# Optimization experiments

Hardware: AMD Instinct MI355X
Metric: run time of the kernel (lower is better)

Reference implementation:

```python
import jax, jax.numpy as jnp
import numpy as np

ND, ED, HD, L, K = 128, 64, 256, 4, 24   # node_dim, edge_dim(num_rbf), hidden_dim, num_layers, max_neighbors
CUTOFF = 8.0
N = 2048  # n_atoms


def _silu(x):
    return x * jax.nn.sigmoid(x)


def _lattice(lengths, angles):
    a, b, c = lengths[0], lengths[1], lengths[2]
    deg = jnp.asarray(np.pi / 180.0, lengths.dtype)
    al, be, ga = angles[0] * deg, angles[1] * deg, angles[2] * deg
    lx = a
    xy = b * jnp.cos(ga)
    xz = c * jnp.cos(be)
    ly = b * jnp.sin(ga)
    yz = (b * c * jnp.cos(al) - xy * xz) / ly
    lz = jnp.sqrt(c ** 2 - xz ** 2 - yz ** 2)
    z = jnp.zeros((), lengths.dtype)
    return jnp.stack([jnp.stack([lx, z, z]), jnp.stack([xy, ly, z]), jnp.stack([xz, yz, lz])])


def _rbf(d):
    centers = jnp.linspace(0.0, CUTOFF, ED)
    widths = jnp.full((ED,), CUTOFF / ED)
    d = d[..., None]
    g = jnp.exp(-(d - centers) ** 2 / (2.0 * widths ** 2))
    cv = 0.5 * (jnp.cos(d * jnp.pi / CUTOFF) + 1.0) * (d < CUTOFF).astype(d.dtype)
    return g * cv


def _forward(atom_types, frac_coords, lengths, angles, timesteps, emb, tW, tb,
             eW1, eb1, eW2, eb2, nW1, nb1, nW2, nb2, cW1, cb1, cW2, cb2):
    n = frac_coords.shape[0]
    lattice = _lattice(lengths, angles)            # [3,3]
    cart = frac_coords @ lattice                   # [n,3]

    # ---- vectorized periodic neighbor graph (replaces host triple loop) ----
    shifts = jnp.asarray(np.array([[i, j, k] for i in (-1, 0, 1) for j in (-1, 0, 1) for k in (-1, 0, 1)],
                                  dtype=np.float32))
    sv = shifts @ lattice                          # [27,3]
    p = cart[None, :, :] + sv[:, None, :]          # [27,n,3] shifted atom positions
    # squared distances without materializing [27,n,n,3]
    d2 = (p * p).sum(-1)[:, :, None] + (cart * cart).sum(-1)[None, None, :] \
         - 2.0 * jnp.einsum('snk,mk->snm', p, cart)      # [27, n_j, n_i]
    dist = jnp.sqrt(jnp.maximum(d2, 1e-12))
    cand = jnp.where((dist < CUTOFF) & (dist > 0.01), dist, jnp.inf)
    cand = cand.reshape(27 * n, n).T               # [n_i, 27*n_j]; flat f = s*n + j
    _, idx = jax.lax.top_k(-cand, K)               # K smallest distances per atom i
    d_k = jnp.take_along_axis(cand, idx, axis=1)   # [n,K]
    dst = (idx % n).reshape(-1)                    # neighbor atom j (edge_list = [i, j])
    src = jnp.repeat(jnp.arange(n), K)             # center atom i
    valid = jnp.isfinite(d_k).reshape(-1)
    m = valid.astype(jnp.float32)[:, None]         # [E,1] pad mask
    d_e = jnp.where(valid, d_k.reshape(-1), 0.0)
    edge_attr = _rbf(d_e)                          # [E, ED]

    # ---- EGNN stack ----
    nf = emb[atom_types] + timesteps @ tW + tb     # [n, ND]
    coords = cart
    seg = lambda x, i: jax.ops.segment_sum(x, i, num_segments=n)
    for l in range(L):
        ef = jnp.concatenate([nf[src], nf[dst], edge_attr], axis=-1)   # [E, 2*ND+ED]
        msg = _silu(_silu(ef @ eW1[l] + eb1[l]) @ eW2[l] + eb2[l])     # [E, HD]
        aggr = seg(msg * m, dst)                                       # [n, HD]
        nf = nf + _silu(jnp.concatenate([nf, aggr], axis=-1) @ nW1[l] + nb1[l]) @ nW2[l] + nb2[l]
        w = _silu(msg @ cW1[l] + cb1[l]) @ cW2[l] + cb2[l]             # [E,1]
        cd = coords[src] - coords[dst]
        cd = cd / (jnp.linalg.norm(cd, axis=-1, keepdims=True) + 1e-8)
        coords = coords + seg(w * cd * m, dst)
    return nf, coords


def setup_inputs() -> dict:
    key = jax.random.key(0)
    ks = jax.random.split(key, 16)
    pr = lambda k, shape: jax.random.normal(k, shape, jnp.float32) * 0.02
    return dict(
        atom_types=jax.random.randint(ks[0], (N,), 0, 100),
        frac_coords=jax.random.uniform(ks[1], (N, 3), jnp.float32),
        lengths=jnp.ones((3,), jnp.float32) * 12.0,
        angles=jnp.ones((3,), jnp.float32) * 90.0,
        timesteps=jax.random.normal(ks[2], (N, 128), jnp.float32),
        emb=pr(ks[3], (100, ND)),
        tW=pr(ks[4], (128, ND)), tb=jnp.zeros((ND,), jnp.float32),
        eW1=pr(ks[5], (L, 2 * ND + ED, HD)), eb1=jnp.zeros((L, HD), jnp.float32),
        eW2=pr(ks[6], (L, HD, HD)), eb2=jnp.zeros((L, HD), jnp.float32),
        nW1=pr(ks[7], (L, ND + HD, HD)), nb1=jnp.zeros((L, HD), jnp.float32),
        nW2=pr(ks[8], (L, HD, ND)), nb2=jnp.zeros((L, ND), jnp.float32),
        cW1=pr(ks[9], (L, HD, HD // 2)), cb1=jnp.zeros((L, HD // 2), jnp.float32),
        cW2=pr(ks[10], (L, HD // 2, 1)), cb2=jnp.zeros((L, 1), jnp.float32),
    )


def reference(atom_types, frac_coords, lengths, angles, timesteps, emb, tW, tb,
              eW1, eb1, eW2, eb2, nW1, nb1, nW2, nb2, cW1, cb1, cW2, cb2):
    return _forward(atom_types, frac_coords, lengths, angles, timesteps, emb, tW, tb,
                    eW1, eb1, eW2, eb2, nW1, nb1, nW2, nb2, cW1, cb1, cW2, cb2)
```

## Files before the change

### kernel.cpp

```cpp
#include <hip/hip_runtime.h>
#include <math.h>

#define NA 2048
#define KN 24
#define NE (NA*KN)
#define NDIM 128
#define EDIM 64
#define HDIM 256
#define NLAYER 4
#define MAXDEG 256

typedef __attribute__((ext_vector_type(8))) short bf16x8;
typedef __attribute__((ext_vector_type(4))) float f32x4;

__device__ __forceinline__ float siluf(float x) { return x / (1.0f + expf(-x)); }
__device__ __forceinline__ ushort f2b(float x) {
    unsigned u = __float_as_uint(x);
    return (ushort)((u + 0x7fffu + ((u >> 16) & 1u)) >> 16);
}
__device__ __forceinline__ float b2f(ushort h) { return __uint_as_float(((unsigned)h) << 16); }

__device__ __forceinline__ void gl_lds(const void* g, void* lds) {
    __builtin_amdgcn_global_load_lds(
        (const __attribute__((address_space(1))) unsigned int*)g,
        (__attribute__((address_space(3))) unsigned int*)lds, 16, 0, 0);
}

struct Lat { float lx, xy, xz, ly, yz, lz; };

__device__ __forceinline__ Lat make_lattice(const float* lengths, const float* angles) {
    const float deg = 0.017453292519943295f;
    float a = lengths[0], b = lengths[1], c = lengths[2];
    float al = angles[0]*deg, be = angles[1]*deg, ga = angles[2]*deg;
    Lat L;
    L.lx = a;
    L.xy = b * cosf(ga);
    L.xz = c * cosf(be);
    L.ly = b * sinf(ga);
    L.yz = (b*c*cosf(al) - L.xy*L.xz) / L.ly;
    L.lz = sqrtf(c*c - L.xz*L.xz - L.yz*L.yz);
    return L;
}

__global__ void setup_kernel(const float* __restrict__ frac, const float* __restrict__ lengths,
                             const float* __restrict__ angles, float* __restrict__ cart,
                             float* __restrict__ cxg, float* __restrict__ cyg,
                             float* __restrict__ czg, float* __restrict__ sv,
                             int* __restrict__ ccnt) {
    int i = blockIdx.x*blockDim.x + threadIdx.x;
    Lat L = make_lattice(lengths, angles);
    if (i < NA) {
        float f0 = frac[i*3], f1 = frac[i*3+1], f2 = frac[i*3+2];
        float x = f0*L.lx + f1*L.xy + f2*L.xz;
        float y = f1*L.ly + f2*L.yz;
        float z = f2*L.lz;
        cart[i*3+0] = x; cart[i*3+1] = y; cart[i*3+2] = z;
        cxg[i] = x; cyg[i] = y; czg[i] = z;
        ccnt[i] = 0;
    }
    if (i < 27) {
        float s0 = (float)(i/9 - 1), s1 = (float)((i/3)%3 - 1), s2 = (float)(i%3 - 1);
        sv[i*3+0] = s0*L.lx + s1*L.xy + s2*L.xz;
        sv[i*3+1] = s1*L.ly + s2*L.yz;
        sv[i*3+2] = s2*L.lz;
    }
}

__global__ __launch_bounds__(64) void knn_kernel(
        const float* __restrict__ cxg, const float* __restrict__ cyg,
        const float* __restrict__ czg, const float* __restrict__ lengths,
        const float* __restrict__ angles, const float* __restrict__ sv,
        int* __restrict__ dstl, ushort* __restrict__ rbf16,
        int* __restrict__ ccnt, int* __restrict__ cedg) {
    __shared__ float sd2L[16][64];
    __shared__ int   sfL[16][64];
    const int lane = threadIdx.x;
    const int i = blockIdx.x;
    Lat L = make_lattice(lengths, angles);
    const float deg = 0.017453292519943295f;
    const bool ortho = fabsf(cosf(angles[0]*deg)) < 1e-6f &&
                       fabsf(cosf(angles[1]*deg)) < 1e-6f &&
                       fabsf(cosf(angles[2]*deg)) < 1e-6f;
    const float cx = cxg[i], cy = cyg[i], cz = czg[i];
    const float invlx = 1.0f/L.lx, invly = 1.0f/L.ly, invlz = 1.0f/L.lz;
    float R = 2.8f;
    int mycnt = 0, cnt = 0;
    bool flatm = false;
    for (int attempt = 0; attempt < 8; ++attempt) {
        const float R2 = R*R;
        mycnt = 0;
        flatm = !ortho || (attempt == 7);
        if (!flatm) {
#pragma unroll 2
            for (int j0 = 0; j0 < NA; j0 += 64) {
                const int j = j0 + lane;
                const float dx = cxg[j] - cx, dy = cyg[j] - cy, dz = czg[j] - cz;
                const float kx = rintf(dx*invlx), ky = rintf(dy*invly), kz = rintf(dz*invlz);
                const float ex = dx - (kx*L.lx + ky*L.xy + kz*L.xz);
                const float ey = dy - (ky*L.ly + kz*L.yz);
                const float ez = dz - kz*L.lz;
                const float d2 = fmaf(ex,ex,fmaf(ey,ey,ez*ez));
                if (d2 < R2 && d2 > 1e-4f) {
                    const int s = (1-(int)kx)*9 + (1-(int)ky)*3 + (1-(int)kz);
                    if (mycnt < 16) { sd2L[mycnt][lane] = d2; sfL[mycnt][lane] = (s<<11) + j; }
                    ++mycnt;
                }
            }
            if (__ballot(mycnt > 16)) {
                flatm = true;
            } else {
                int tot = mycnt;
                for (int off = 32; off > 0; off >>= 1) tot += __shfl_xor(tot, off, 64);
                cnt = tot;
            }
        }
        if (flatm) {
            cnt = 0;
            for (int s = 0; s < 27; ++s) {
                const float svx = sv[s*3], svy = sv[s*3+1], svz = sv[s*3+2];
                for (int j0 = 0; j0 < NA; j0 += 64) {
                    const int j = j0 + lane;
                    const float ex = cxg[j] + svx - cx;
                    const float ey = cyg[j] + svy - cy;
                    const float ez = czg[j] + svz - cz;
                    const float d2 = fmaf(ex,ex,fmaf(ey,ey,ez*ez));
                    const bool hit = (d2 < R2) && (d2 > 1e-4f);
                    const unsigned long long m = __ballot(hit);
                    const int rank = __popcll(m & ((1ull<<lane)-1ull));
                    const int slot = cnt + rank;
                    if (hit && slot < 1024) { sd2L[slot>>6][slot&63] = d2; sfL[slot>>6][slot&63] = (s<<11)+j; }
                    cnt += __popcll(m);
                }
            }
            cnt = min(cnt, 1024);
        }
        if (cnt >= KN) break;
        R = fminf(R*1.6f, flatm ? 8.0f : 5.9f);
    }
    int vq;
    if (flatm) vq = (lane < cnt) ? min(16, ((cnt - 1 - lane) >> 6) + 1) : 0;
    else       vq = mycnt;
    unsigned long long key[16];
#pragma unroll
    for (int q = 0; q < 16; ++q) {
        const float d2v = sd2L[q][lane];
        const int fl = sfL[q][lane];
        const unsigned long long kk = ((unsigned long long)__float_as_uint(d2v) << 20)
                                    | ((unsigned long long)(unsigned)fl << 4) | (unsigned)q;
        key[q] = (q < vq) ? kk : ~0ull;
    }
    float der[KN];
    for (int k = 0; k < KN; ++k) {
        unsigned long long lm = key[0];
#pragma unroll
        for (int q = 1; q < 16; ++q) lm = key[q] < lm ? key[q] : lm;
        for (int off = 32; off > 0; off >>= 1) {
            unsigned long long o = __shfl_xor(lm, off, 64);
            lm = o < lm ? o : lm;
        }
        der[k] = sqrtf(__uint_as_float((unsigned)(lm >> 20)));
        if (lane == 0) {
            const int jn = (int)((lm >> 4) & 2047u);
            dstl[i*KN + k] = jn;
            const int slot = atomicAdd(&ccnt[jn], 1);
            if (slot < MAXDEG) cedg[(size_t)jn*MAXDEG + slot] = i*KN + k;
        }
#pragma unroll
        for (int q = 0; q < 16; ++q) if (key[q] == lm) key[q] = ~0ull;
    }
    const float center = (8.0f/63.0f) * (float)lane;
    for (int k = 0; k < KN; ++k) {
        const float d = der[k];
        const float diff = d - center;
        const float g = expf(diff*diff * -32.0f);
        const float cv = 0.5f * (cosf(d * (float)(M_PI/8.0)) + 1.0f);
        rbf16[(size_t)(i*KN + k)*EDIM + lane] = f2b(g * cv);
    }
}

__global__ void csort_kernel(const int* __restrict__ ccnt, int* __restrict__ cedg) {
    const int j = blockIdx.x*4 + (threadIdx.x >> 6);
    const int lane = threadIdx.x & 63;
    const int cnt = min(ccnt[j], MAXDEG);
    if (cnt <= 64) {
        int v = (lane < cnt) ? cedg[(size_t)j*MAXDEG + lane] : 0x7FFFFFFF;
#pragma unroll
        for (int k = 2; k <= 64; k <<= 1) {
#pragma unroll
            for (int s = k >> 1; s > 0; s >>= 1) {
                int o = __shfl_xor(v, s, 64);
                const bool up = ((lane & k) == 0);
                const bool lowhalf = ((lane & s) == 0);
                v = ((lowhalf == up) ? min(v, o) : max(v, o));
            }
        }
        if (lane < cnt) cedg[(size_t)j*MAXDEG + lane] = v;
    } else if (lane == 0) {
        int* L = cedg + (size_t)j*MAXDEG;
        for (int a = 1; a < cnt; ++a) {
            int v = L[a]; int b = a - 1;
            while (b >= 0 && L[b] > v) { L[b+1] = L[b]; --b; }
            L[b+1] = v;
        }
    }
}

__global__ void nf_init_kernel(const int* __restrict__ atom_types, const float* __restrict__ ts,
                               const float* __restrict__ emb, const float* __restrict__ tW,
                               const float* __restrict__ tb, float* __restrict__ nf,
                               ushort* __restrict__ nf16) {
    int i = blockIdx.x, c = threadIdx.x;
    float acc = emb[atom_types[i]*NDIM + c] + tb[c];
    for (int kk = 0; kk < 128; ++kk) acc += ts[i*128 + kk] * tW[kk*NDIM + c];
    nf[i*NDIM + c] = acc;
    nf16[i*NDIM + c] = f2b(acc);
}

__global__ void wprep_all(const float* __restrict__ eW1, const float* __restrict__ eW2,
                          const float* __restrict__ cW1, const float* __restrict__ nW1,
                          const float* __restrict__ nW2,
                          ushort* __restrict__ eW1t, ushort* __restrict__ eW2t,
                          ushort* __restrict__ cW1t, ushort* __restrict__ nW1t,
                          ushort* __restrict__ nW2t) {
    __shared__ float tile[64][65];
    const int b = blockIdx.x;
    const float* W; ushort* Wt; int Kk, Nn, rel;
    if (b < 80)       { W = eW1; Wt = eW1t; Kk = 320; Nn = 256; rel = b; }
    else if (b < 144) { W = eW2; Wt = eW2t; Kk = 256; Nn = 256; rel = b - 80; }
    else if (b < 176) { W = cW1; Wt = cW1t; Kk = 256; Nn = 128; rel = b - 144; }
    else if (b < 272) { W = nW1; Wt = nW1t; Kk = 384; Nn = 256; rel = b - 176; }
    else              { W = nW2; Wt = nW2t; Kk = 256; Nn = 128; rel = b - 272; }
    const int kt = Kk >> 6, nt = Nn >> 6, per = kt*nt;
    const int l = rel / per, r2 = rel - l*per;
    const int k0 = (r2 / nt) * 64, n0 = (r2 - (r2/nt)*nt) * 64;
    const float* Wl = W + (size_t)l*Kk*Nn;
    ushort* Wtl = Wt + (size_t)l*Kk*Nn;
    const int tr = threadIdx.x >> 6, tc = threadIdx.x & 63;
#pragma unroll
    for (int q = 0; q < 16; ++q) {
        const int k = q*4 + tr;
        tile[k][tc] = Wl[(size_t)(k0 + k)*Nn + n0 + tc];
    }
    __syncthreads();
#pragma unroll
    for (int q = 0; q < 16; ++q) {
        const int n = q*4 + tr;
        Wtl[(size_t)(n0 + n)*Kk + k0 + tc] = f2b(tile[tc][n]);
    }
}

__global__ __launch_bounds__(256) void edge_fused(
        const ushort* __restrict__ nf16, const int* __restrict__ dstl,
        const ushort* __restrict__ rbf16,
        const ushort* __restrict__ eW1t,
        const ushort* __restrict__ eW2t,
        const ushort* __restrict__ cW1t,
        const float* __restrict__ eb1, const float* __restrict__ eb2,
        const float* __restrict__ cb1, const float* __restrict__ cW2v,
        const float* __restrict__ cb2v,
        ushort* __restrict__ msg16, float* __restrict__ wvout) {
    __shared__ alignas(16) char R0[40960];
    __shared__ alignas(16) char R1[32768];
    __shared__ int sdst[64];
    __shared__ float wred[2][64];
    ushort* As = (ushort*)R0;
    ushort* Bs = (ushort*)(R0 + 8192);
    ushort* B2 = (ushort*)R1;
    ushort* Cs = (ushort*)R1;

    const int t = threadIdx.x, wave = t >> 6, lane = t & 63;
    const int row0 = blockIdx.x*64;
    if (t < 64) sdst[t] = dstl[row0 + t];
    __syncthreads();
    const int wr = (wave >> 1)*32;
    const int wcB = (wave & 1)*128;
    const int lr = lane & 15, g0 = lane >> 4;

    auto STAGEA = [&](int buf, int k0) {
        {
            const int r = wave*16 + (lane >> 2);
            const int g = (lane & 3) ^ ((r >> 1) & 3);
            const int kg = k0 + g*8;
            const int e = row0 + r;
            const ushort* gp;
            if (kg < NDIM)        gp = nf16 + (size_t)(e/KN)*NDIM + kg;
            else if (kg < 2*NDIM) gp = nf16 + (size_t)sdst[r]*NDIM + (kg - NDIM);
            else                  gp = rbf16 + (size_t)e*EDIM + (kg - 2*NDIM);
            gl_lds(gp, As + (size_t)buf*2048 + (wave*16)*32);
        }
#pragma unroll
        for (int q = 0; q < 4; ++q) {
            const int rowb = wave*64 + q*16 + (lane >> 2);
            const int g = (lane & 3) ^ ((rowb >> 1) & 3);
            gl_lds(eW1t + (size_t)rowb*320 + k0 + g*8,
                   Bs + (size_t)buf*8192 + (wave*64 + q*16)*32);
        }
    };
    f32x4 acc[2][8];
#pragma unroll
    for (int m = 0; m < 2; ++m)
#pragma unroll
        for (int n = 0; n < 8; ++n) acc[m][n] = (f32x4){0.f,0.f,0.f,0.f};
    STAGEA(0, 0);
    int cur = 0;
    for (int it = 0; it < 10; ++it) {
        if (it + 1 < 10) {
            STAGEA(cur ^ 1, (it + 1)*32);
            asm volatile("s_waitcnt vmcnt(5)" ::: "memory");
        } else {
            asm volatile("s_waitcnt vmcnt(0)" ::: "memory");
        }
        __builtin_amdgcn_sched_barrier(0);
        __builtin_amdgcn_s_barrier();
        __builtin_amdgcn_sched_barrier(0);
        bf16x8 af[2], bfr[8];
#pragma unroll
        for (int m = 0; m < 2; ++m) {
            const int rA = wr + m*16 + lr;
            af[m] = *reinterpret_cast<const bf16x8*>(&As[cur*2048 + rA*32 + ((g0 ^ ((rA>>1)&3)))*8]);
        }
#pragma unroll
        for (int n = 0; n < 8; ++n) {
            const int rB = wcB + n*16 + lr;
            bfr[n] = *reinterpret_cast<const bf16x8*>(&Bs[(size_t)cur*8192 + rB*32 + ((g0 ^ ((rB>>1)&3)))*8]);
        }
#pragma unroll
        for (int m = 0; m < 2; ++m)
#pragma unroll
            for (int n = 0; n < 8; ++n)
                acc[m][n] = __builtin_amdgcn_mfma_f32_16x16x32_bf16(af[m], bfr[n], acc[m][n], 0, 0, 0);
        asm volatile("s_waitcnt lgkmcnt(0)" ::: "memory");
        __builtin_amdgcn_sched_barrier(0);
        __builtin_amdgcn_s_barrier();
        __builtin_amdgcn_sched_barrier(0);
        cur ^= 1;
    }
#pragma unroll
    for (int n = 0; n < 8; ++n) {
        const int cc = wcB + n*16 + lr;
        const float b1 = eb1[cc];
#pragma unroll
        for (int m = 0; m < 2; ++m) {
#pragma unroll
            for (int j = 0; j < 4; ++j) {
                const int rr = wr + m*16 + g0*4 + j;
                const float x = siluf(acc[m][n][j] + b1);
                *(ushort*)(R0 + rr*512 + ((cc*2) ^ ((rr&7)<<4))) = f2b(x);
            }
        }
    }
    __syncthreads();

#pragma unroll
    for (int m = 0; m < 2; ++m)
#pragma unroll
        for (int n = 0; n < 8; ++n) acc[m][n] = (f32x4){0.f,0.f,0.f,0.f};
    auto STAGEB = [&](int buf, int k0) {
#pragma unroll
        for (int q = 0; q < 4; ++q) {
            const int rowb = wave*64 + q*16 + (lane >> 2);
            const int g = (lane & 3) ^ ((rowb >> 1) & 3);
            gl_lds(eW2t + (size_t)rowb*256 + k0 + g*8,
                   B2 + (size_t)buf*8192 + (wave*64 + q*16)*32);
        }
    };
    STAGEB(0, 0);
    cur = 0;
    for (int it = 0; it < 8; ++it) {
        if (it + 1 < 8) {
            STAGEB(cur ^ 1, (it + 1)*32);
            asm volatile("s_waitcnt vmcnt(4)" ::: "memory");
        } else {
            asm volatile("s_waitcnt vmcnt(0)" ::: "memory");
        }
        __builtin_amdgcn_sched_barrier(0);
        __builtin_amdgcn_s_barrier();
        __builtin_amdgcn_sched_barrier(0);
        bf16x8 af[2], bfr[8];
#pragma unroll
        for (int m = 0; m < 2; ++m) {
            const int rA = wr + m*16 + lr;
            const int kc = it*4 + g0;
            af[m] = *reinterpret_cast<const bf16x8*>(R0 + rA*512 + ((kc*16) ^ ((rA&7)<<4)));
        }
#pragma unroll
        for (int n = 0; n < 8; ++n) {
            const int rB = wcB + n*16 + lr;
            bfr[n] = *reinterpret_cast<const bf16x8*>(&B2[(size_t)cur*8192 + rB*32 + ((g0 ^ ((rB>>1)&3)))*8]);
        }
#pragma unroll
        for (int m = 0; m < 2; ++m)
#pragma unroll
            for (int n = 0; n < 8; ++n)
                acc[m][n] = __builtin_amdgcn_mfma_f32_16x16x32_bf16(af[m], bfr[n], acc[m][n], 0, 0, 0);
        asm volatile("s_waitcnt lgkmcnt(0)" ::: "memory");
        __builtin_amdgcn_sched_barrier(0);
        __builtin_amdgcn_s_barrier();
        __builtin_amdgcn_sched_barrier(0);
        cur ^= 1;
    }
#pragma unroll
    for (int n = 0; n < 8; ++n) {
        const int cc = wcB + n*16 + lr;
        const float b2 = eb2[cc];
#pragma unroll
        for (int m = 0; m < 2; ++m) {
#pragma unroll
            for (int j = 0; j < 4; ++j) {
                const int rr = wr + m*16 + g0*4 + j;
                const ushort h = f2b(siluf(acc[m][n][j] + b2));
                msg16[(size_t)(row0 + rr)*256 + cc] = h;
                *(ushort*)(R0 + rr*512 + ((cc*2) ^ ((rr&7)<<4))) = h;
            }
        }
    }
    __syncthreads();

    const int wcC = (wave & 1)*64;
    f32x4 acc3[2][4];
#pragma unroll
    for (int m = 0; m < 2; ++m)
#pragma unroll
        for (int n = 0; n < 4; ++n) acc3[m][n] = (f32x4){0.f,0.f,0.f,0.f};
    auto STAGEC = [&](int buf, int k0) {
#pragma unroll
        for (int q = 0; q < 2; ++q) {
            const int rowb = wave*32 + q*16 + (lane >> 2);
            const int g = (lane & 3) ^ ((rowb >> 1) & 3);
            gl_lds(cW1t + (size_t)rowb*256 + k0 + g*8,
                   Cs + (size_t)buf*4096 + (wave*32 + q*16)*32);
        }
    };
    STAGEC(0, 0);
    cur = 0;
    for (int it = 0; it < 8; ++it) {
        if (it + 1 < 8) {
            STAGEC(cur ^ 1, (it + 1)*32);
            asm volatile("s_waitcnt vmcnt(2)" ::: "memory");
        } else {
            asm volatile("s_waitcnt vmcnt(0)" ::: "memory");
        }
        __builtin_amdgcn_sched_barrier(0);
        __builtin_amdgcn_s_barrier();
        __builtin_amdgcn_sched_barrier(0);
        bf16x8 af[2], bfr[4];
#pragma unroll
        for (int m = 0; m < 2; ++m) {
            const int rA = wr + m*16 + lr;
            const int kc = it*4 + g0;
            af[m] = *reinterpret_cast<const bf16x8*>(R0 + rA*512 + ((kc*16) ^ ((rA&7)<<4)));
        }
#pragma unroll
        for (int n = 0; n < 4; ++n) {
            const int rB = wcC + n*16 + lr;
            bfr[n] = *reinterpret_cast<const bf16x8*>(&Cs[(size_t)cur*4096 + rB*32 + ((g0 ^ ((rB>>1)&3)))*8]);
        }
#pragma unroll
        for (int m = 0; m < 2; ++m)
#pragma unroll
            for (int n = 0; n < 4; ++n)
                acc3[m][n] = __builtin_amdgcn_mfma_f32_16x16x32_bf16(af[m], bfr[n], acc3[m][n], 0, 0, 0);
        asm volatile("s_waitcnt lgkmcnt(0)" ::: "memory");
        __builtin_amdgcn_sched_barrier(0);
        __builtin_amdgcn_s_barrier();
        __builtin_amdgcn_sched_barrier(0);
        cur ^= 1;
    }
    float part[2][4];
#pragma unroll
    for (int m = 0; m < 2; ++m)
#pragma unroll
        for (int j = 0; j < 4; ++j) part[m][j] = 0.0f;
#pragma unroll
    for (int n = 0; n < 4; ++n) {
        const int cc = wcC + n*16 + lr;
        const float bb = cb1[cc];
        const float cw = cW2v[cc];
#pragma unroll
        for (int m = 0; m < 2; ++m)
#pragma unroll
            for (int j = 0; j < 4; ++j)
                part[m][j] += siluf(acc3[m][n][j] + bb) * cw;
    }
#pragma unroll
    for (int off = 1; off < 16; off <<= 1)
#pragma unroll
        for (int m = 0; m < 2; ++m)
#pragma unroll
            for (int j = 0; j < 4; ++j)
                part[m][j] += __shfl_xor(part[m][j], off, 64);
    if (lr == 0) {
#pragma unroll
        for (int m = 0; m < 2; ++m)
#pragma unroll
            for (int j = 0; j < 4; ++j)
                wred[wave & 1][wr + m*16 + g0*4 + j] = part[m][j];
    }
    __syncthreads();
    if (t < 64) wvout[row0 + t] = wred[0][t] + wred[1][t] + cb2v[0];
}

template<int AMODE, int EPI>
__global__ __launch_bounds__(256) void bgemm_kernel(
        const ushort* __restrict__ A, const ushort* __restrict__ nf16,
        const ushort* __restrict__ aggr16, const ushort* __restrict__ Bt,
        const float* __restrict__ bias, const float* __restrict__ res,
        float* __restrict__ Cf, ushort* __restrict__ C16, int M, int Nn, int Kk) {
    __shared__ alignas(16) ushort As[2][128*32];
    __shared__ alignas(16) ushort Bs[2][128*32];
    const int t = threadIdx.x;
    const int wave = t >> 6, lane = t & 63;
    const int row0 = blockIdx.x*128, col0 = blockIdx.y*128;
    const int wr = (wave >> 1)*64, wc = (wave & 1)*64;
    const int lr = lane & 15, g0 = lane >> 4;

    auto STAGE = [&](int buf, int k0) {
#pragma unroll
        for (int q = 0; q < 4; ++q) {
            const int rbase = (q & 1)*64 + wave*16;
            const int r = rbase + (lane >> 2);
            const int g = (lane & 3) ^ ((r >> 1) & 3);
            const int kg = k0 + g*8;
            const int ldsbase = rbase * 32;
            if (q < 2) {
                const ushort* gp;
                if (AMODE == 0) {
                    gp = A + (size_t)(row0 + r)*Kk + kg;
                } else {
                    const int e = row0 + r;
                    if (kg < NDIM) gp = nf16 + (size_t)e*NDIM + kg;
                    else           gp = aggr16 + (size_t)e*HDIM + (kg - NDIM);
                }
                gl_lds(gp, &As[buf][ldsbase]);
            } else {
                gl_lds(Bt + (size_t)(col0 + r)*Kk + kg, &Bs[buf][ldsbase]);
            }
        }
    };

    f32x4 acc[4][4] = {};
    const int nk = Kk >> 5;
    STAGE(0, 0);
    int cur = 0;
    for (int it = 0; it < nk; ++it) {
        if (it + 1 < nk) {
            STAGE(cur ^ 1, (it + 1) << 5);
            asm volatile("s_waitcnt vmcnt(4)" ::: "memory");
        } else {
            asm volatile("s_waitcnt vmcnt(0)" ::: "memory");
        }
        __builtin_amdgcn_sched_barrier(0);
        __builtin_amdgcn_s_barrier();
        __builtin_amdgcn_sched_barrier(0);
        bf16x8 af[4], bfr[4];
#pragma unroll
        for (int m = 0; m < 4; ++m) {
            const int rA = wr + m*16 + lr;
            af[m] = *reinterpret_cast<const bf16x8*>(&As[cur][rA*32 + (g0 ^ ((rA>>1)&3))*8]);
        }
#pragma unroll
        for (int n = 0; n < 4; ++n) {
            const int rB = wc + n*16 + lr;
            bfr[n] = *reinterpret_cast<const bf16x8*>(&Bs[cur][rB*32 + (g0 ^ ((rB>>1)&3))*8]);
        }
#pragma unroll
        for (int m = 0; m < 4; ++m)
#pragma unroll
            for (int n = 0; n < 4; ++n)
                acc[m][n] = __builtin_amdgcn_mfma_f32_16x16x32_bf16(af[m], bfr[n], acc[m][n], 0, 0, 0);
        asm volatile("s_waitcnt lgkmcnt(0)" ::: "memory");
        __builtin_amdgcn_sched_barrier(0);
        __builtin_amdgcn_s_barrier();
        __builtin_amdgcn_sched_barrier(0);
        cur ^= 1;
    }

#pragma unroll
    for (int n = 0; n < 4; ++n) {
        const int cc = col0 + wc + n*16 + lr;
        const float bb = bias[cc];
#pragma unroll
        for (int m = 0; m < 4; ++m) {
#pragma unroll
            for (int j = 0; j < 4; ++j) {
                const int rr = row0 + wr + m*16 + (lane >> 4)*4 + j;
                float x = acc[m][n][j] + bb;
                if constexpr (EPI == 0) {
                    C16[(size_t)rr*Nn + cc] = f2b(siluf(x));
                } else {
                    x += res[(size_t)rr*Nn + cc];
                    Cf[(size_t)rr*Nn + cc] = x;
                    C16[(size_t)rr*Nn + cc] = f2b(x);
                }
            }
        }
    }
}

__global__ void aggr_kernel(const ushort* __restrict__ msg16, const int* __restrict__ ccnt,
                            const int* __restrict__ cedg, ushort* __restrict__ aggr16) {
    __shared__ int se[4][64];
    const int w = threadIdx.x >> 6, lane = threadIdx.x & 63;
    const int j = blockIdx.x*4 + w;
    const int cnt = min(ccnt[j], MAXDEG);
    se[w][lane] = (lane < cnt) ? cedg[(size_t)j*MAXDEG + lane] : 0;
    __syncthreads();
    const int c4 = lane*4;
    float s0 = 0, s1 = 0, s2 = 0, s3 = 0;
    const int lim = min(cnt, 64);
    for (int q = 0; q < lim; ++q) {
        const int e = se[w][q];
        ushort4 v = *reinterpret_cast<const ushort4*>(&msg16[(size_t)e*HDIM + c4]);
        s0 += b2f(v.x); s1 += b2f(v.y); s2 += b2f(v.z); s3 += b2f(v.w);
    }
    for (int q = 64; q < cnt; ++q) {
        const int e = cedg[(size_t)j*MAXDEG + q];
        ushort4 v = *reinterpret_cast<const ushort4*>(&msg16[(size_t)e*HDIM + c4]);
        s0 += b2f(v.x); s1 += b2f(v.y); s2 += b2f(v.z); s3 += b2f(v.w);
    }
    ushort4 o; o.x = f2b(s0); o.y = f2b(s1); o.z = f2b(s2); o.w = f2b(s3);
    *reinterpret_cast<ushort4*>(&aggr16[(size_t)j*HDIM + c4]) = o;
}

__global__ void coords_kernel(const float* __restrict__ cold, const float* __restrict__ wv,
                              const int* __restrict__ ccnt, const int* __restrict__ cedg,
                              float* __restrict__ cnew) {
    const int w = threadIdx.x >> 6, lane = threadIdx.x & 63;
    const int j = blockIdx.x*4 + w;
    const int cnt = min(ccnt[j], MAXDEG);
    const float jx = cold[j*3], jy = cold[j*3+1], jz = cold[j*3+2];
    float dx = 0, dy = 0, dz = 0;
    for (int q = lane; q < cnt; q += 64) {
        const int e = cedg[(size_t)j*MAXDEG + q];
        const int si = e / KN;
        const float ax = cold[si*3]   - jx;
        const float ay = cold[si*3+1] - jy;
        const float az = cold[si*3+2] - jz;
        const float inv = wv[e] / (sqrtf(ax*ax + ay*ay + az*az) + 1e-8f);
        dx += inv*ax; dy += inv*ay; dz += inv*az;
    }
    for (int off = 32; off > 0; off >>= 1) {
        dx += __shfl_xor(dx, off, 64);
        dy += __shfl_xor(dy, off, 64);
        dz += __shfl_xor(dz, off, 64);
    }
    if (lane == 0) {
        cnew[j*3]   = jx + dx;
        cnew[j*3+1] = jy + dy;
        cnew[j*3+2] = jz + dz;
    }
}

__global__ void copyout_kernel(const float* __restrict__ nf, const float* __restrict__ coords,
                               float* __restrict__ out) {
    int idx = blockIdx.x*256 + threadIdx.x;
    if (idx < NA*NDIM) out[idx] = nf[idx];
    else if (idx < NA*NDIM + NA*3) out[idx] = coords[idx - NA*NDIM];
}

extern "C" void kernel_launch(void* const* d_in, const int* in_sizes, int n_in,
                              void* d_out, int out_size, void* d_ws, size_t ws_size,
                              hipStream_t stream) {
    const int*   atom_types = (const int*)  d_in[0];
    const float* frac       = (const float*)d_in[1];
    const float* lengths    = (const float*)d_in[2];
    const float* angles     = (const float*)d_in[3];
    const float* timesteps  = (const float*)d_in[4];
    const float* emb        = (const float*)d_in[5];
    const float* tW         = (const float*)d_in[6];
    const float* tb         = (const float*)d_in[7];
    const float* eW1        = (const float*)d_in[8];
    const float* eb1        = (const float*)d_in[9];
    const float* eW2        = (const float*)d_in[10];
    const float* eb2        = (const float*)d_in[11];
    const float* nW1        = (const float*)d_in[12];
    const float* nb1        = (const float*)d_in[13];
    const float* nW2        = (const float*)d_in[14];
    const float* nb2        = (const float*)d_in[15];
    const float* cW1        = (const float*)d_in[16];
    const float* cb1        = (const float*)d_in[17];
    const float* cW2        = (const float*)d_in[18];
    const float* cb2        = (const float*)d_in[19];

    char* p = (char*)d_ws;
    auto alloc = [&](size_t bytes) { char* q = p; p += (bytes + 255) & ~(size_t)255; return q; };
    float*  sv    = (float*) alloc(81*4);
    float*  c0    = (float*) alloc((size_t)NA*3*4);
    float*  c1    = (float*) alloc((size_t)NA*3*4);
    float*  cxg   = (float*) alloc((size_t)NA*4);
    float*  cyg   = (float*) alloc((size_t)NA*4);
    float*  czg   = (float*) alloc((size_t)NA*4);
    float*  nf    = (float*) alloc((size_t)NA*NDIM*4);
    int*    dstl  = (int*)   alloc((size_t)NE*4);
    ushort* rbf16 = (ushort*)alloc((size_t)NE*EDIM*2);
    int*    ccnt  = (int*)   alloc((size_t)NA*4);
    int*    cedg  = (int*)   alloc((size_t)NA*MAXDEG*4);
    ushort* aggr16= (ushort*)alloc((size_t)NA*HDIM*2);
    ushort* t116  = (ushort*)alloc((size_t)NA*HDIM*2);
    float*  wv    = (float*) alloc((size_t)NE*4);
    ushort* nf16  = (ushort*)alloc((size_t)NA*NDIM*2);
    ushort* msg16 = (ushort*)alloc((size_t)NE*HDIM*2);
    ushort* eW1t  = (ushort*)alloc((size_t)NLAYER*(2*NDIM+EDIM)*HDIM*2);
    ushort* eW2t  = (ushort*)alloc((size_t)NLAYER*HDIM*HDIM*2);
    ushort* cW1t  = (ushort*)alloc((size_t)NLAYER*(HDIM/2)*HDIM*2);
    ushort* nW1t  = (ushort*)alloc((size_t)NLAYER*(NDIM+HDIM)*HDIM*2);
    ushort* nW2t  = (ushort*)alloc((size_t)NLAYER*HDIM*NDIM*2);

    setup_kernel<<<8, 256, 0, stream>>>(frac, lengths, angles, c0, cxg, cyg, czg, sv, ccnt);
    knn_kernel<<<NA, 64, 0, stream>>>(cxg, cyg, czg, lengths, angles, sv,
                                      dstl, rbf16, ccnt, cedg);
    csort_kernel<<<NA/4, 256, 0, stream>>>(ccnt, cedg);
    nf_init_kernel<<<NA, 128, 0, stream>>>(atom_types, timesteps, emb, tW, tb, nf, nf16);
    wprep_all<<<304, 256, 0, stream>>>(eW1, eW2, cW1, nW1, nW2,
                                       eW1t, eW2t, cW1t, nW1t, nW2t);

    float* cin = c0; float* cout = c1;
    for (int l = 0; l < NLAYER; ++l) {
        const float* eb1l = eb1 + (size_t)l*HDIM;
        const float* eb2l = eb2 + (size_t)l*HDIM;
        const float* nb1l = nb1 + (size_t)l*HDIM;
        const float* nb2l = nb2 + (size_t)l*NDIM;
        const float* cb1l = cb1 + (size_t)l*(HDIM/2);
        const float* cW2l = cW2 + (size_t)l*(HDIM/2);
        const float* cb2l = cb2 + (size_t)l;

        edge_fused<<<NE/64, 256, 0, stream>>>(
            nf16, dstl, rbf16,
            eW1t + (size_t)l*(2*NDIM+EDIM)*HDIM, eW2t + (size_t)l*HDIM*HDIM,
            cW1t + (size_t)l*(HDIM/2)*HDIM,
            eb1l, eb2l, cb1l, cW2l, cb2l, msg16, wv);
        aggr_kernel<<<NA/4, 256, 0, stream>>>(msg16, ccnt, cedg, aggr16);
        bgemm_kernel<2,0><<<dim3(NA/128, HDIM/128), 256, 0, stream>>>(
            nullptr, nf16, aggr16, nW1t + (size_t)l*(NDIM+HDIM)*HDIM, nb1l, nullptr,
            nullptr, t116, NA, HDIM, NDIM+HDIM);
        bgemm_kernel<0,2><<<dim3(NA/128, NDIM/128), 256, 0, stream>>>(
            t116, nullptr, nullptr, nW2t + (size_t)l*HDIM*NDIM, nb2l, nf,
            nf, nf16, NA, NDIM, HDIM);
        coords_kernel<<<NA/4, 256, 0, stream>>>(cin, wv, ccnt, cedg, cout);
        float* tmp = cin; cin = cout; cout = tmp;
    }
    copyout_kernel<<<(NA*NDIM + NA*3)/256, 256, 0, stream>>>(nf, cin, (float*)d_out);
}
```

Measured before the change: 418.1 us.

## Enlarge edge_fused tile to 96 edges and restructure LDS and staging

Raises the edge tile per block from 64 to 96 rows, so each wave computes three 16-row MFMA slabs and every weight tile loaded into LDS is reused across more edges. The LDS regions are remapped, and the first weight tile of the next GEMM stage is prefetched while the previous epilogue runs. msg16 is now written with coalesced 16-byte stores from the swizzled LDS tile instead of scattered 2-byte stores, and s_setprio is raised around the MFMA blocks. In exchange it uses more LDS and registers (possible occupancy loss), balances A-loads unevenly across waves, and launches fewer blocks.

After: 467.4 us. +11.8%, slower.

```diff
diff --git a/kernel.cpp b/kernel.cpp
--- a/kernel.cpp
+++ b/kernel.cpp
@@ -9,6 +9,7 @@
 #define HDIM 256
 #define NLAYER 4
 #define MAXDEG 256
+#define EB 96
 
 typedef __attribute__((ext_vector_type(8))) short bf16x8;
 typedef __attribute__((ext_vector_type(4))) float f32x4;
@@ -259,26 +260,29 @@
         const float* __restrict__ cb1, const float* __restrict__ cW2v,
         const float* __restrict__ cb2v,
         ushort* __restrict__ msg16, float* __restrict__ wvout) {
-    __shared__ alignas(16) char R0[40960];
+    __shared__ alignas(16) char R0[49152];
     __shared__ alignas(16) char R1[32768];
-    __shared__ int sdst[64];
-    __shared__ float wred[2][64];
-    ushort* As = (ushort*)R0;
-    ushort* Bs = (ushort*)(R0 + 8192);
+    ushort* Bs = (ushort*)R0;
+    int*    sdst = (int*)(R0 + 32768);
+    ushort* As = (ushort*)R1;
     ushort* B2 = (ushort*)R1;
     ushort* Cs = (ushort*)R1;
+    float*  wredp = (float*)R1;
 
     const int t = threadIdx.x, wave = t >> 6, lane = t & 63;
-    const int row0 = blockIdx.x*64;
-    if (t < 64) sdst[t] = dstl[row0 + t];
+    const int row0 = blockIdx.x*EB;
+    if (t < EB) sdst[t] = dstl[row0 + t];
     __syncthreads();
-    const int wr = (wave >> 1)*32;
+    const int wr = (wave >> 1)*48;
     const int wcB = (wave & 1)*128;
     const int lr = lane & 15, g0 = lane >> 4;
 
     auto STAGEA = [&](int buf, int k0) {
-        {
-            const int r = wave*16 + (lane >> 2);
+        const int na = (wave < 2) ? 2 : 1;
+        const int a0 = (wave < 2) ? wave*2 : wave + 2;
+        for (int q = 0; q < na; ++q) {
+            const int grp = a0 + q;
+            const int r = grp*16 + (lane >> 2);
             const int g = (lane & 3) ^ ((r >> 1) & 3);
             const int kg = k0 + g*8;
             const int e = row0 + r;
@@ -286,7 +290,7 @@
             if (kg < NDIM)        gp = nf16 + (size_t)(e/KN)*NDIM + kg;
             else if (kg < 2*NDIM) gp = nf16 + (size_t)sdst[r]*NDIM + (kg - NDIM);
             else                  gp = rbf16 + (size_t)e*EDIM + (kg - 2*NDIM);
-            gl_lds(gp, As + (size_t)buf*2048 + (wave*16)*32);
+            gl_lds(gp, As + (size_t)buf*3072 + grp*512);
         }
 #pragma unroll
         for (int q = 0; q < 4; ++q) {
@@ -296,9 +300,9 @@
                    Bs + (size_t)buf*8192 + (wave*64 + q*16)*32);
         }
     };
-    f32x4 acc[2][8];
-#pragma unroll
-    for (int m = 0; m < 2; ++m)
+    f32x4 acc[3][8];
+#pragma unroll
+    for (int m = 0; m < 3; ++m)
 #pragma unroll
         for (int n = 0; n < 8; ++n) acc[m][n] = (f32x4){0.f,0.f,0.f,0.f};
     STAGEA(0, 0);
@@ -306,41 +310,53 @@
     for (int it = 0; it < 10; ++it) {
         if (it + 1 < 10) {
             STAGEA(cur ^ 1, (it + 1)*32);
-            asm volatile("s_waitcnt vmcnt(5)" ::: "memory");
+            if (wave < 2) asm volatile("s_waitcnt vmcnt(6)" ::: "memory");
+            else          asm volatile("s_waitcnt vmcnt(5)" ::: "memory");
         } else {
             asm volatile("s_waitcnt vmcnt(0)" ::: "memory");
         }
         __builtin_amdgcn_sched_barrier(0);
         __builtin_amdgcn_s_barrier();
         __builtin_amdgcn_sched_barrier(0);
-        bf16x8 af[2], bfr[8];
-#pragma unroll
-        for (int m = 0; m < 2; ++m) {
+        bf16x8 af[3], bfr[8];
+#pragma unroll
+        for (int m = 0; m < 3; ++m) {
             const int rA = wr + m*16 + lr;
-            af[m] = *reinterpret_cast<const bf16x8*>(&As[cur*2048 + rA*32 + ((g0 ^ ((rA>>1)&3)))*8]);
+            af[m] = *reinterpret_cast<const bf16x8*>(&As[cur*3072 + rA*32 + ((g0 ^ ((rA>>1)&3)))*8]);
         }
 #pragma unroll
         for (int n = 0; n < 8; ++n) {
             const int rB = wcB + n*16 + lr;
             bfr[n] = *reinterpret_cast<const bf16x8*>(&Bs[(size_t)cur*8192 + rB*32 + ((g0 ^ ((rB>>1)&3)))*8]);
         }
-#pragma unroll
-        for (int m = 0; m < 2; ++m)
+        __builtin_amdgcn_s_setprio(1);
+#pragma unroll
+        for (int m = 0; m < 3; ++m)
 #pragma unroll
             for (int n = 0; n < 8; ++n)
                 acc[m][n] = __builtin_amdgcn_mfma_f32_16x16x32_bf16(af[m], bfr[n], acc[m][n], 0, 0, 0);
+        __builtin_amdgcn_s_setprio(0);
         asm volatile("s_waitcnt lgkmcnt(0)" ::: "memory");
         __builtin_amdgcn_sched_barrier(0);
         __builtin_amdgcn_s_barrier();
         __builtin_amdgcn_sched_barrier(0);
         cur ^= 1;
+    }
+    {
+#pragma unroll
+        for (int q = 0; q < 4; ++q) {
+            const int rowb = wave*64 + q*16 + (lane >> 2);
+            const int g = (lane & 3) ^ ((rowb >> 1) & 3);
+            gl_lds(eW2t + (size_t)rowb*256 + g*8,
+                   B2 + (wave*64 + q*16)*32);
+        }
     }
 #pragma unroll
     for (int n = 0; n < 8; ++n) {
         const int cc = wcB + n*16 + lr;
         const float b1 = eb1[cc];
 #pragma unroll
-        for (int m = 0; m < 2; ++m) {
+        for (int m = 0; m < 3; ++m) {
 #pragma unroll
             for (int j = 0; j < 4; ++j) {
                 const int rr = wr + m*16 + g0*4 + j;
@@ -352,7 +368,7 @@
     __syncthreads();
 
 #pragma unroll
-    for (int m = 0; m < 2; ++m)
+    for (int m = 0; m < 3; ++m)
 #pragma unroll
         for (int n = 0; n < 8; ++n) acc[m][n] = (f32x4){0.f,0.f,0.f,0.f};
     auto STAGEB = [&](int buf, int k0) {
@@ -364,7 +380,6 @@
                    B2 + (size_t)buf*8192 + (wave*64 + q*16)*32);
         }
     };
-    STAGEB(0, 0);
     cur = 0;
     for (int it = 0; it < 8; ++it) {
         if (it + 1 < 8) {
@@ -376,9 +391,9 @@
         __builtin_amdgcn_sched_barrier(0);
         __builtin_amdgcn_s_barrier();
         __builtin_amdgcn_sched_barrier(0);
-        bf16x8 af[2], bfr[8];
-#pragma unroll
-        for (int m = 0; m < 2; ++m) {
+        bf16x8 af[3], bfr[8];
+#pragma unroll
+        for (int m = 0; m < 3; ++m) {
             const int rA = wr + m*16 + lr;
             const int kc = it*4 + g0;
             af[m] = *reinterpret_cast<const bf16x8*>(R0 + rA*512 + ((kc*16) ^ ((rA&7)<<4)));
@@ -388,38 +403,47 @@
             const int rB = wcB + n*16 + lr;
             bfr[n] = *reinterpret_cast<const bf16x8*>(&B2[(size_t)cur*8192 + rB*32 + ((g0 ^ ((rB>>1)&3)))*8]);
         }
-#pragma unroll
-        for (int m = 0; m < 2; ++m)
+        __builtin_amdgcn_s_setprio(1);
+#pragma unroll
+        for (int m = 0; m < 3; ++m)
 #pragma unroll
             for (int n = 0; n < 8; ++n)
                 acc[m][n] = __builtin_amdgcn_mfma_f32_16x16x32_bf16(af[m], bfr[n], acc[m][n], 0, 0, 0);
+        __builtin_amdgcn_s_setprio(0);
         asm volatile("s_waitcnt lgkmcnt(0)" ::: "memory");
         __builtin_amdgcn_sched_barrier(0);
         __builtin_amdgcn_s_barrier();
         __builtin_amdgcn_sched_barrier(0);
         cur ^= 1;
+    }
+    {
+#pragma unroll
+        for (int q = 0; q < 2; ++q) {
+            const int rowb = wave*32 + q*16 + (lane >> 2);
+            const int g = (lane & 3) ^ ((rowb >> 1) & 3);
+            gl_lds(cW1t + (size_t)rowb*256 + g*8,
+                   Cs + (wave*32 + q*16)*32);
+        }
     }
 #pragma unroll
     for (int n = 0; n < 8; ++n) {
         const int cc = wcB + n*16 + lr;
         const float b2 = eb2[cc];
 #pragma unroll
-        for (int m = 0; m < 2; ++m) {
+        for (int m = 0; m < 3; ++m) {
 #pragma unroll
             for (int j = 0; j < 4; ++j) {
                 const int rr = wr + m*16 + g0*4 + j;
-                const ushort h = f2b(siluf(acc[m][n][j] + b2));
-                msg16[(size_t)(row0 + rr)*256 + cc] = h;
-                *(ushort*)(R0 + rr*512 + ((cc*2) ^ ((rr&7)<<4))) = h;
+                *(ushort*)(R0 + rr*512 + ((cc*2) ^ ((rr&7)<<4))) = f2b(siluf(acc[m][n][j] + b2));
             }
         }
     }
     __syncthreads();
 
     const int wcC = (wave & 1)*64;
-    f32x4 acc3[2][4];
-#pragma unroll
-    for (int m = 0; m < 2; ++m)
+    f32x4 acc3[3][4];
+#pragma unroll
+    for (int m = 0; m < 3; ++m)
 #pragma unroll
         for (int n = 0; n < 4; ++n) acc3[m][n] = (f32x4){0.f,0.f,0.f,0.f};
     auto STAGEC = [&](int buf, int k0) {
@@ -431,7 +455,6 @@
                    Cs + (size_t)buf*4096 + (wave*32 + q*16)*32);
         }
     };
-    STAGEC(0, 0);
     cur = 0;
     for (int it = 0; it < 8; ++it) {
         if (it + 1 < 8) {
@@ -443,9 +466,9 @@
         __builtin_amdgcn_sched_barrier(0);
         __builtin_amdgcn_s_barrier();
         __builtin_amdgcn_sched_barrier(0);
-        bf16x8 af[2], bfr[4];
-#pragma unroll
-        for (int m = 0; m < 2; ++m) {
+        bf16x8 af[3], bfr[4];
+#pragma unroll
+        for (int m = 0; m < 3; ++m) {
             const int rA = wr + m*16 + lr;
             const int kc = it*4 + g0;
             af[m] = *reinterpret_cast<const bf16x8*>(R0 + rA*512 + ((kc*16) ^ ((rA&7)<<4)));
@@ -455,20 +478,22 @@
             const int rB = wcC + n*16 + lr;
             bfr[n] = *reinterpret_cast<const bf16x8*>(&Cs[(size_t)cur*4096 + rB*32 + ((g0 ^ ((rB>>1)&3)))*8]);
         }
-#pragma unroll
-        for (int m = 0; m < 2; ++m)
+        __builtin_amdgcn_s_setprio(1);
+#pragma unroll
+        for (int m = 0; m < 3; ++m)
 #pragma unroll
             for (int n = 0; n < 4; ++n)
                 acc3[m][n] = __builtin_amdgcn_mfma_f32_16x16x32_bf16(af[m], bfr[n], acc3[m][n], 0, 0, 0);
+        __builtin_amdgcn_s_setprio(0);
         asm volatile("s_waitcnt lgkmcnt(0)" ::: "memory");
         __builtin_amdgcn_sched_barrier(0);
         __builtin_amdgcn_s_barrier();
         __builtin_amdgcn_sched_barrier(0);
         cur ^= 1;
     }
-    float part[2][4];
-#pragma unroll
-    for (int m = 0; m < 2; ++m)
+    float part[3][4];
+#pragma unroll
+    for (int m = 0; m < 3; ++m)
 #pragma unroll
         for (int j = 0; j < 4; ++j) part[m][j] = 0.0f;
 #pragma unroll
@@ -477,7 +502,7 @@
         const float bb = cb1[cc];
         const float cw = cW2v[cc];
 #pragma unroll
-        for (int m = 0; m < 2; ++m)
+        for (int m = 0; m < 3; ++m)
 #pragma unroll
             for (int j = 0; j < 4; ++j)
                 part[m][j] += siluf(acc3[m][n][j] + bb) * cw;
@@ -485,19 +510,27 @@
 #pragma unroll
     for (int off = 1; off < 16; off <<= 1)
 #pragma unroll
-        for (int m = 0; m < 2; ++m)
+        for (int m = 0; m < 3; ++m)
 #pragma unroll
             for (int j = 0; j < 4; ++j)
                 part[m][j] += __shfl_xor(part[m][j], off, 64);
     if (lr == 0) {
 #pragma unroll
-        for (int m = 0; m < 2; ++m)
+        for (int m = 0; m < 3; ++m)
 #pragma unroll
             for (int j = 0; j < 4; ++j)
-                wred[wave & 1][wr + m*16 + g0*4 + j] = part[m][j];
+                wredp[(wave & 1)*EB + wr + m*16 + g0*4 + j] = part[m][j];
     }
     __syncthreads();
-    if (t < 64) wvout[row0 + t] = wred[0][t] + wred[1][t] + cb2v[0];
+    if (t < EB) wvout[row0 + t] = wredp[t] + wredp[EB + t] + cb2v[0];
+#pragma unroll
+    for (int k = 0; k < 12; ++k) {
+        const int off = (t + k*256) * 16;
+        const int row = off >> 9;
+        const int cg = ((off >> 4) & 31) ^ (row & 7);
+        uint4 v = *reinterpret_cast<const uint4*>(R0 + off);
+        *reinterpret_cast<uint4*>(msg16 + (size_t)(row0 + row)*256 + cg*8) = v;
+    }
 }
 
 template<int AMODE, int EPI>
@@ -724,7 +757,7 @@
         const float* cW2l = cW2 + (size_t)l*(HDIM/2);
         const float* cb2l = cb2 + (size_t)l;
 
-        edge_fused<<<NE/64, 256, 0, stream>>>(
+        edge_fused<<<NE/EB, 256, 0, stream>>>(
             nf16, dstl, rbf16,
             eW1t + (size_t)l*(2*NDIM+EDIM)*HDIM, eW2t + (size_t)l*HDIM*HDIM,
             cW1t + (size_t)l*(HDIM/2)*HDIM,
```

## Prefetch next GEMM weights early, coalesce msg stores, fuse aggr and coords kernels

Applied to the files above, without the earlier changes.

In the fused edge kernel, the first weight tiles for the second and third GEMMs are now issued right after the previous GEMM loop, before the epilogue runs. This lets the global loads overlap with the SiLU/bf16 conversion. The message tile is written to global memory with coalesced 16-byte stores from the swizzled LDS copy, replacing scattered 2-byte stores. MFMA blocks are wrapped in s_setprio, and the aggregation and coordinate-update kernels are merged into one node kernel that reuses the edge list cached in LDS, removing a launch per layer. The risk is that weight prefetches into R1/Cs could overlap buffers still being read, which is a correctness hazard if the aliasing is wrong.

Result: faster. 407.4 us (-2.6%).

```diff
diff --git a/kernel.cpp b/kernel.cpp
--- a/kernel.cpp
+++ b/kernel.cpp
@@ -9,6 +9,7 @@
 #define HDIM 256
 #define NLAYER 4
 #define MAXDEG 256
+#define EB 64
 
 typedef __attribute__((ext_vector_type(8))) short bf16x8;
 typedef __attribute__((ext_vector_type(4))) float f32x4;
@@ -269,8 +270,8 @@
     ushort* Cs = (ushort*)R1;
 
     const int t = threadIdx.x, wave = t >> 6, lane = t & 63;
-    const int row0 = blockIdx.x*64;
-    if (t < 64) sdst[t] = dstl[row0 + t];
+    const int row0 = blockIdx.x*EB;
+    if (t < EB) sdst[t] = dstl[row0 + t];
     __syncthreads();
     const int wr = (wave >> 1)*32;
     const int wcB = (wave & 1)*128;
@@ -324,16 +325,27 @@
             const int rB = wcB + n*16 + lr;
             bfr[n] = *reinterpret_cast<const bf16x8*>(&Bs[(size_t)cur*8192 + rB*32 + ((g0 ^ ((rB>>1)&3)))*8]);
         }
+        __builtin_amdgcn_s_setprio(1);
 #pragma unroll
         for (int m = 0; m < 2; ++m)
 #pragma unroll
             for (int n = 0; n < 8; ++n)
                 acc[m][n] = __builtin_amdgcn_mfma_f32_16x16x32_bf16(af[m], bfr[n], acc[m][n], 0, 0, 0);
+        __builtin_amdgcn_s_setprio(0);
         asm volatile("s_waitcnt lgkmcnt(0)" ::: "memory");
         __builtin_amdgcn_sched_barrier(0);
         __builtin_amdgcn_s_barrier();
         __builtin_amdgcn_sched_barrier(0);
         cur ^= 1;
+    }
+    {
+#pragma unroll
+        for (int q = 0; q < 4; ++q) {
+            const int rowb = wave*64 + q*16 + (lane >> 2);
+            const int g = (lane & 3) ^ ((rowb >> 1) & 3);
+            gl_lds(eW2t + (size_t)rowb*256 + g*8,
+                   B2 + (wave*64 + q*16)*32);
+        }
     }
 #pragma unroll
     for (int n = 0; n < 8; ++n) {
@@ -364,7 +376,6 @@
                    B2 + (size_t)buf*8192 + (wave*64 + q*16)*32);
         }
     };
-    STAGEB(0, 0);
     cur = 0;
     for (int it = 0; it < 8; ++it) {
         if (it + 1 < 8) {
@@ -388,16 +399,27 @@
             const int rB = wcB + n*16 + lr;
             bfr[n] = *reinterpret_cast<const bf16x8*>(&B2[(size_t)cur*8192 + rB*32 + ((g0 ^ ((rB>>1)&3)))*8]);
         }
+        __builtin_amdgcn_s_setprio(1);
 #pragma unroll
         for (int m = 0; m < 2; ++m)
 #pragma unroll
             for (int n = 0; n < 8; ++n)
                 acc[m][n] = __builtin_amdgcn_mfma_f32_16x16x32_bf16(af[m], bfr[n], acc[m][n], 0, 0, 0);
+        __builtin_amdgcn_s_setprio(0);
         asm volatile("s_waitcnt lgkmcnt(0)" ::: "memory");
         __builtin_amdgcn_sched_barrier(0);
         __builtin_amdgcn_s_barrier();
         __builtin_amdgcn_sched_barrier(0);
         cur ^= 1;
+    }
+    {
+#pragma unroll
+        for (int q = 0; q < 2; ++q) {
+            const int rowb = wave*32 + q*16 + (lane >> 2);
+            const int g = (lane & 3) ^ ((rowb >> 1) & 3);
+            gl_lds(cW1t + (size_t)rowb*256 + g*8,
+                   Cs + (wave*32 + q*16)*32);
+        }
     }
 #pragma unroll
     for (int n = 0; n < 8; ++n) {
@@ -408,9 +430,7 @@
 #pragma unroll
             for (int j = 0; j < 4; ++j) {
                 const int rr = wr + m*16 + g0*4 + j;
-                const ushort h = f2b(siluf(acc[m][n][j] + b2));
-                msg16[(size_t)(row0 + rr)*256 + cc] = h;
-                *(ushort*)(R0 + rr*512 + ((cc*2) ^ ((rr&7)<<4))) = h;
+                *(ushort*)(R0 + rr*512 + ((cc*2) ^ ((rr&7)<<4))) = f2b(siluf(acc[m][n][j] + b2));
             }
         }
     }
@@ -431,7 +451,6 @@
                    Cs + (size_t)buf*4096 + (wave*32 + q*16)*32);
         }
     };
-    STAGEC(0, 0);
     cur = 0;
     for (int it = 0; it < 8; ++it) {
         if (it + 1 < 8) {
@@ -455,11 +474,13 @@
             const int rB = wcC + n*16 + lr;
             bfr[n] = *reinterpret_cast<const bf16x8*>(&Cs[(size_t)cur*4096 + rB*32 + ((g0 ^ ((rB>>1)&3)))*8]);
         }
+        __builtin_amdgcn_s_setprio(1);
 #pragma unroll
         for (int m = 0; m < 2; ++m)
 #pragma unroll
             for (int n = 0; n < 4; ++n)
                 acc3[m][n] = __builtin_amdgcn_mfma_f32_16x16x32_bf16(af[m], bfr[n], acc3[m][n], 0, 0, 0);
+        __builtin_amdgcn_s_setprio(0);
         asm volatile("s_waitcnt lgkmcnt(0)" ::: "memory");
         __builtin_amdgcn_sched_barrier(0);
         __builtin_amdgcn_s_barrier();
@@ -497,7 +518,15 @@
                 wred[wave & 1][wr + m*16 + g0*4 + j] = part[m][j];
     }
     __syncthreads();
-    if (t < 64) wvout[row0 + t] = wred[0][t] + wred[1][t] + cb2v[0];
+    if (t < EB) wvout[row0 + t] = wred[0][t] + wred[1][t] + cb2v[0];
+#pragma unroll
+    for (int k = 0; k < 8; ++k) {
+        const int off = (t + k*256) * 16;
+        const int row = off >> 9;
+        const int cg = ((off >> 4) & 31) ^ (row & 7);
+        uint4 v = *reinterpret_cast<const uint4*>(R0 + off);
+        *reinterpret_cast<uint4*>(msg16 + (size_t)(row0 + row)*256 + cg*8) = v;
+    }
 }
 
 template<int AMODE, int EPI>
@@ -597,8 +626,10 @@
     }
 }
 
-__global__ void aggr_kernel(const ushort* __restrict__ msg16, const int* __restrict__ ccnt,
-                            const int* __restrict__ cedg, ushort* __restrict__ aggr16) {
+__global__ void node_kernel(const ushort* __restrict__ msg16, const float* __restrict__ cold,
+                            const float* __restrict__ wv, const int* __restrict__ ccnt,
+                            const int* __restrict__ cedg,
+                            ushort* __restrict__ aggr16, float* __restrict__ cnew) {
     __shared__ int se[4][64];
     const int w = threadIdx.x >> 6, lane = threadIdx.x & 63;
     const int j = blockIdx.x*4 + w;
@@ -620,18 +651,10 @@
     }
     ushort4 o; o.x = f2b(s0); o.y = f2b(s1); o.z = f2b(s2); o.w = f2b(s3);
     *reinterpret_cast<ushort4*>(&aggr16[(size_t)j*HDIM + c4]) = o;
-}
-
-__global__ void coords_kernel(const float* __restrict__ cold, const float* __restrict__ wv,
-                              const int* __restrict__ ccnt, const int* __restrict__ cedg,
-                              float* __restrict__ cnew) {
-    const int w = threadIdx.x >> 6, lane = threadIdx.x & 63;
-    const int j = blockIdx.x*4 + w;
-    const int cnt = min(ccnt[j], MAXDEG);
     const float jx = cold[j*3], jy = cold[j*3+1], jz = cold[j*3+2];
     float dx = 0, dy = 0, dz = 0;
     for (int q = lane; q < cnt; q += 64) {
-        const int e = cedg[(size_t)j*MAXDEG + q];
+        const int e = (q < 64) ? se[w][q] : cedg[(size_t)j*MAXDEG + q];
         const int si = e / KN;
         const float ax = cold[si*3]   - jx;
         const float ay = cold[si*3+1] - jy;
@@ -724,19 +747,18 @@
         const float* cW2l = cW2 + (size_t)l*(HDIM/2);
         const float* cb2l = cb2 + (size_t)l;
 
-        edge_fused<<<NE/64, 256, 0, stream>>>(
+        edge_fused<<<NE/EB, 256, 0, stream>>>(
             nf16, dstl, rbf16,
             eW1t + (size_t)l*(2*NDIM+EDIM)*HDIM, eW2t + (size_t)l*HDIM*HDIM,
             cW1t + (size_t)l*(HDIM/2)*HDIM,
             eb1l, eb2l, cb1l, cW2l, cb2l, msg16, wv);
-        aggr_kernel<<<NA/4, 256, 0, stream>>>(msg16, ccnt, cedg, aggr16);
+        node_kernel<<<NA/4, 256, 0, stream>>>(msg16, cin, wv, ccnt, cedg, aggr16, cout);
         bgemm_kernel<2,0><<<dim3(NA/128, HDIM/128), 256, 0, stream>>>(
             nullptr, nf16, aggr16, nW1t + (size_t)l*(NDIM+HDIM)*HDIM, nb1l, nullptr,
             nullptr, t116, NA, HDIM, NDIM+HDIM);
         bgemm_kernel<0,2><<<dim3(NA/128, NDIM/128), 256, 0, stream>>>(
             t116, nullptr, nullptr, nW2t + (size_t)l*HDIM*NDIM, nb2l, nf,
             nf, nf16, NA, NDIM, HDIM);
-        coords_kernel<<<NA/4, 256, 0, stream>>>(cin, wv, ccnt, cedg, cout);
         float* tmp = cin; cin = cout; cout = tmp;
     }
     copyout_kernel<<<(NA*NDIM + NA*3)/256, 256, 0, stream>>>(nf, cin, (float*)d_out);
```
